# Performance work log

Measured on AMD Instinct MI355X. Metric: run time of the kernel, lower is better.

The kernel has to match this reference:

```python
import jax, jax.numpy as jnp
import numpy as np

N_HEADS = 16


def setup_inputs() -> dict:
    key = jax.random.key(0)
    k1, k2, k3, k4 = jax.random.split(key, 4)
    B, T, C = 2, 2048, 1024
    x = jax.random.normal(k1, (B, T, C), dtype=jnp.float32)
    scale = 1.0 / np.sqrt(C)
    Wq = jax.random.normal(k2, (C, C), dtype=jnp.float32) * scale
    Wk = jax.random.normal(k3, (C, C), dtype=jnp.float32) * scale
    Wv = jax.random.normal(k4, (C, C), dtype=jnp.float32) * scale
    return {"x": x, "Wq": Wq, "Wk": Wk, "Wv": Wv}


def reference(x, Wq, Wk, Wv):
    B, T, C = x.shape
    H = N_HEADS
    Dh = C // H
    # Faithful to original: direct view of (B,T,C) -> (B,H,T,Dh) (no transpose)
    q = (x @ Wq.T).reshape(B, H, T, Dh)
    k = (x @ Wk.T).reshape(B, H, T, Dh)
    v = (x @ Wv.T).reshape(B, H, T, Dh)
    scores = jnp.einsum('bhqd,bhkd->bhqk', q, k) * (1.0 / (Dh ** 0.5))
    mask = jnp.tril(jnp.ones((T, T), dtype=bool))  # causal mask
    scores = jnp.where(mask, scores, -jnp.inf)
    att = jax.nn.softmax(scores, axis=-1)
    out = jnp.einsum('bhqk,bhkd->bhqd', att, v)
    return out.reshape(B, T, C)
```

## Files before the change

### kernel.cpp

```cpp
#include <hip/hip_runtime.h>
#include <hip/hip_bf16.h>
#include <stdint.h>

#define AS1 __attribute__((address_space(1)))
#define AS3 __attribute__((address_space(3)))

typedef __bf16 bf16x8 __attribute__((ext_vector_type(8)));
typedef float  f32x4  __attribute__((ext_vector_type(4)));
typedef unsigned short ushort8v __attribute__((ext_vector_type(8)));
typedef unsigned short ushort4v __attribute__((ext_vector_type(4)));
typedef short short8v __attribute__((ext_vector_type(8)));
typedef short short4v __attribute__((ext_vector_type(4)));

__device__ __forceinline__ unsigned short f2bf(float f) {
    unsigned int u = __float_as_uint(f);
    u += 0x7fffu + ((u >> 16) & 1u);
    return (unsigned short)(u >> 16);
}
__device__ __forceinline__ unsigned int pk2bf(float a, float b) {
    __hip_bfloat162 h = __float22bfloat162_rn(make_float2(a, b));
    unsigned int u;
    __builtin_memcpy(&u, &h, 4);
    return u;
}
__device__ __forceinline__ void g2lds16(const void* gp, void* lp) {
    __builtin_amdgcn_global_load_lds((AS1 void*)gp, (AS3 void*)lp, 16, 0, 0);
}
#define E2(x) __builtin_amdgcn_exp2f(x)

__global__ __launch_bounds__(256) void cast_all(const float* __restrict__ x,
                                                const float* __restrict__ w0,
                                                const float* __restrict__ w1,
                                                const float* __restrict__ w2,
                                                unsigned short* __restrict__ xb,
                                                unsigned short* __restrict__ wc) {
    int id = blockIdx.x;
    const float* s;
    unsigned short* d;
    int base;
    if (id < 4096) { s = x; d = xb; base = id; }
    else {
        int z = (id - 4096) >> 10;
        s = (z == 0) ? w0 : (z == 1) ? w1 : w2;
        d = wc + (size_t)z * 1048576;
        base = (id - 4096) & 1023;
    }
    int i = (base * 256 + threadIdx.x) * 4;
    float4 v = *(const float4*)(s + i);
    ushort4v o = { f2bf(v.x), f2bf(v.y), f2bf(v.z), f2bf(v.w) };
    *(ushort4v*)(d + i) = o;
}

__global__ __launch_bounds__(256) void gemm_qkv(const unsigned short* __restrict__ X,
                                                const unsigned short* __restrict__ W,
                                                unsigned short* __restrict__ QKV) {
    const int K = 1024, N = 1024;
    const int z = blockIdx.z;
    const unsigned short* A = X;
    const unsigned short* B = W + (size_t)z * (1024 * 1024);
    unsigned short* C = QKV + (size_t)z * (4096 * 1024);
    const float qs = (z == 0) ? 0.18033688011112042f : 1.0f;

    const int m0 = blockIdx.y * 128;
    const int n0 = blockIdx.x * 128;

    __shared__ unsigned short As[128 * 32];
    __shared__ unsigned short Bs[128 * 32];

    const int t = threadIdx.x;
    const int w = t >> 6;
    const int l = t & 63;
    const int wm = (w >> 1) * 64;
    const int wn = (w & 1) * 64;
    const int cl = l & 15;
    const int quad = l >> 4;

    const int srow = w * 16 + (l >> 2);
    const int scol = (l & 3) * 8;

    f32x4 acc[4][4] = {};

    for (int k0 = 0; k0 < K; k0 += 32) {
        g2lds16(A + (size_t)(m0 + srow) * K + k0 + scol,      As + w * 512);
        g2lds16(A + (size_t)(m0 + 64 + srow) * K + k0 + scol, As + 2048 + w * 512);
        g2lds16(B + (size_t)(n0 + srow) * K + k0 + scol,      Bs + w * 512);
        g2lds16(B + (size_t)(n0 + 64 + srow) * K + k0 + scol, Bs + 2048 + w * 512);
        __syncthreads();

        bf16x8 af[4], bfr[4];
        #pragma unroll
        for (int i = 0; i < 4; ++i)
            af[i] = *(const bf16x8*)(As + (wm + i * 16 + cl) * 32 + quad * 8);
        #pragma unroll
        for (int j = 0; j < 4; ++j)
            bfr[j] = *(const bf16x8*)(Bs + (wn + j * 16 + cl) * 32 + quad * 8);
        #pragma unroll
        for (int i = 0; i < 4; ++i)
            #pragma unroll
            for (int j = 0; j < 4; ++j)
                acc[i][j] = __builtin_amdgcn_mfma_f32_16x16x32_bf16(af[i], bfr[j], acc[i][j], 0, 0, 0);
        __syncthreads();
    }

    #pragma unroll
    for (int i = 0; i < 4; ++i) {
        #pragma unroll
        for (int r = 0; r < 4; ++r) {
            size_t row = (size_t)(m0 + wm + i * 16 + quad * 4 + r);
            #pragma unroll
            for (int j = 0; j < 4; ++j)
                C[row * N + (n0 + wn + j * 16 + cl)] = f2bf(acc[i][j][r] * qs);
        }
    }
}

__global__ __launch_bounds__(256) void vtrans(const unsigned short* __restrict__ Vn,
                                              unsigned short* __restrict__ V3) {
    const int bh = blockIdx.y;
    const int T0 = blockIdx.x * 128;
    __shared__ unsigned short L[128 * 72];
    const int t = threadIdx.x;

    const unsigned short* src = Vn + (size_t)bh * 131072 + (size_t)T0 * 64;
    #pragma unroll
    for (int p = 0; p < 4; ++p) {
        int r = p * 32 + (t >> 3), c = (t & 7) * 8;
        *(ushort8v*)(L + r * 72 + c) = *(const ushort8v*)(src + (size_t)r * 64 + c);
    }
    __syncthreads();
    unsigned short* dst = V3 + (size_t)bh * 131072 + (size_t)(T0 >> 4) * 1024;
    #pragma unroll
    for (int p = 0; p < 2; ++p) {
        int item = p * 256 + t;
        int kb = item >> 6, cl = (item >> 2) & 15, qk = item & 3;
        ushort8v a, b;
        #pragma unroll
        for (int u = 0; u < 8; ++u) {
            int dt = u >> 2, j = u & 3;
            a[u] = L[(kb * 16 + qk * 4 + j) * 72 + dt * 16 + cl];
            b[u] = L[(kb * 16 + qk * 4 + j) * 72 + (dt + 2) * 16 + cl];
        }
        unsigned short* dp = dst + kb * 1024 + cl * 64 + qk * 16;
        *(ushort8v*)(dp) = a;
        *(ushort8v*)(dp + 8) = b;
    }
}

__global__ __launch_bounds__(256) void attn(const unsigned short* __restrict__ QK,
                                            const unsigned short* __restrict__ V3,
                                            float* __restrict__ Out) {
    const int id = blockIdx.x;
    const int bh = (id & 7) * 4 + ((id >> 3) & 3);
    const int pp = id >> 5;
    const int t = threadIdx.x;
    const int w = t >> 6;
    const int l = t & 63;
    const int cl = l & 15;
    const int quad = l >> 4;
    const int c7 = cl & 7;

    const size_t bhoff = (size_t)bh * 131072;
    const unsigned short* Qb = QK + bhoff;
    const unsigned short* Kb = QK + (size_t)4194304 + bhoff;
    const unsigned short* Vb = V3 + bhoff;
    float* Ob = Out + bhoff;

    __shared__ unsigned short KVs[2][8192];

    const int sg0 = t, sg1 = 256 + t;
    const int kO0 = (sg0 >> 3) * 64 + (((sg0 & 7) ^ ((sg0 >> 3) & 7)) * 8);
    const int kO1 = (sg1 >> 3) * 64 + (((sg1 & 7) ^ ((sg1 >> 3) & 7)) * 8);
    const int wg0 = sg0 & 63, wg1 = sg1 & 63;
    const int vO0 = (sg0 >> 6) * 512 + ((wg0 ^ ((wg0 >> 3) & 7)) * 8);
    const int vO1 = (sg1 >> 6) * 512 + ((wg1 ^ ((wg1 >> 3) & 7)) * 8);
    const int lB0 = w * 512;
    const int lB1 = 2048 + w * 512;

    const int oK0 = cl * 64 + (((quad)     ^ c7) * 8);
    const int oK1 = cl * 64 + (((quad + 4) ^ c7) * 8);
    const int oV0 = cl * 64 + (((quad * 2)     ^ c7) * 8);
    const int oV1 = cl * 64 + (((quad * 2 + 1) ^ c7) * 8);

    const int mrel = w * 16 + cl;

    #pragma unroll 1
    for (int hb = 0; hb < 2; ++hb) {
        const int bb = hb ? (31 - pp) : pp;
        const int m0 = bb * 64 + w * 16;
        const int nch = bb + 1;

        bf16x8 qf0, qf1;
        {
            const unsigned short* qa = Qb + (size_t)(m0 + cl) * 64 + quad * 8;
            qf0 = *(const bf16x8*)(qa);
            qf1 = *(const bf16x8*)(qa + 32);
        }

        f32x4 o[4] = {};
        float lps = 0.f;

        {
            unsigned short* s = &KVs[0][0];
            g2lds16(Kb + kO0, s + lB0);
            g2lds16(Kb + kO1, s + lB1);
            g2lds16(Vb + vO0, s + 4096 + lB0);
            g2lds16(Vb + vO1, s + 4096 + lB1);
        }

        for (int c = 0; c < nch; ++c) {
            __syncthreads();
            if (c + 1 < nch) {
                const unsigned short* kg = Kb + (size_t)(c + 1) * 4096;
                const unsigned short* vg = Vb + (size_t)(c + 1) * 4096;
                unsigned short* s = &KVs[(c + 1) & 1][0];
                g2lds16(kg + kO0, s + lB0);
                g2lds16(kg + kO1, s + lB1);
                g2lds16(vg + vO0, s + 4096 + lB0);
                g2lds16(vg + vO1, s + 4096 + lB1);
            }
            const unsigned short* Kl = &KVs[c & 1][0];
            const unsigned short* Vl = Kl + 4096;
            const bool masked = (c == nch - 1) && (hb == 0 ? true : true) && (c == bb);

            bf16x8 kf0[4], kf1[4];
            #pragma unroll
            for (int kt = 0; kt < 4; ++kt) {
                kf0[kt] = *(const bf16x8*)(Kl + kt * 1024 + oK0);
                kf1[kt] = *(const bf16x8*)(Kl + kt * 1024 + oK1);
            }
            f32x4 st[4] = {};
            #pragma unroll
            for (int kt = 0; kt < 4; ++kt) {
                st[kt] = __builtin_amdgcn_mfma_f32_16x16x32_bf16(kf0[kt], qf0, st[kt], 0, 0, 0);
                st[kt] = __builtin_amdgcn_mfma_f32_16x16x32_bf16(kf1[kt], qf1, st[kt], 0, 0, 0);
            }

            short4v pb[4];
            #pragma unroll
            for (int kt = 0; kt < 4; ++kt) {
                float p0, p1, p2, p3;
                if (masked) {
                    const int lk = kt * 16 + quad * 4;
                    p0 = (lk     <= mrel) ? E2(st[kt][0]) : 0.f;
                    p1 = (lk + 1 <= mrel) ? E2(st[kt][1]) : 0.f;
                    p2 = (lk + 2 <= mrel) ? E2(st[kt][2]) : 0.f;
                    p3 = (lk + 3 <= mrel) ? E2(st[kt][3]) : 0.f;
                } else {
                    p0 = E2(st[kt][0]);
                    p1 = E2(st[kt][1]);
                    p2 = E2(st[kt][2]);
                    p3 = E2(st[kt][3]);
                }
                lps += (p0 + p1) + (p2 + p3);
                uint2 u = { pk2bf(p0, p1), pk2bf(p2, p3) };
                short4v pv;
                __builtin_memcpy(&pv, &u, 8);
                pb[kt] = pv;
            }

            #pragma unroll
            for (int kt = 0; kt < 4; ++kt) {
                short8v v0 = *(const short8v*)(Vl + kt * 1024 + oV0);
                short8v v1 = *(const short8v*)(Vl + kt * 1024 + oV1);
                short4v a0 = __builtin_shufflevector(v0, v0, 0, 1, 2, 3);
                short4v a1 = __builtin_shufflevector(v0, v0, 4, 5, 6, 7);
                short4v a2 = __builtin_shufflevector(v1, v1, 0, 1, 2, 3);
                short4v a3 = __builtin_shufflevector(v1, v1, 4, 5, 6, 7);
                o[0] = __builtin_amdgcn_mfma_f32_16x16x16bf16_1k(a0, pb[kt], o[0], 0, 0, 0);
                o[1] = __builtin_amdgcn_mfma_f32_16x16x16bf16_1k(a1, pb[kt], o[1], 0, 0, 0);
                o[2] = __builtin_amdgcn_mfma_f32_16x16x16bf16_1k(a2, pb[kt], o[2], 0, 0, 0);
                o[3] = __builtin_amdgcn_mfma_f32_16x16x16bf16_1k(a3, pb[kt], o[3], 0, 0, 0);
            }
        }
        __syncthreads();

        lps += __shfl_xor(lps, 16);
        lps += __shfl_xor(lps, 32);
        const float inv = 1.0f / lps;
        #pragma unroll
        for (int dt = 0; dt < 4; ++dt) {
            f32x4 r = o[dt];
            r[0] *= inv; r[1] *= inv; r[2] *= inv; r[3] *= inv;
            *(f32x4*)(Ob + (size_t)(m0 + cl) * 64 + dt * 16 + quad * 4) = r;
        }
    }
}

extern "C" void kernel_launch(void* const* d_in, const int* in_sizes, int n_in,
                              void* d_out, int out_size, void* d_ws, size_t ws_size,
                              hipStream_t stream) {
    const float* x  = (const float*)d_in[0];
    const float* Wq = (const float*)d_in[1];
    const float* Wk = (const float*)d_in[2];
    const float* Wv = (const float*)d_in[3];
    float* out = (float*)d_out;

    unsigned short* xb  = (unsigned short*)d_ws;
    unsigned short* wc  = xb + (size_t)4096 * 1024;
    unsigned short* qkv = wc + (size_t)3 * 1024 * 1024;
    unsigned short* vt  = qkv + (size_t)3 * 4096 * 1024;

    hipLaunchKernelGGL(cast_all, dim3(7168), dim3(256), 0, stream, x, Wq, Wk, Wv, xb, wc);
    hipLaunchKernelGGL(gemm_qkv, dim3(8, 32, 3), dim3(256), 0, stream, xb, wc, qkv);
    hipLaunchKernelGGL(vtrans, dim3(16, 32), dim3(256), 0, stream, qkv + (size_t)2 * 4096 * 1024, vt);
    hipLaunchKernelGGL(attn, dim3(512), dim3(256), 0, stream, qkv, vt, out);
}
```

Measured before the change: 148.0 us.

## Double-buffer QKV GEMM with swizzled LDS and share K/V tiles across paired query blocks

The QKV GEMM now double-buffers its LDS tiles, prefetching the next K slice while computing the current one, and XOR-swizzles the LDS column layout to cut bank conflicts. This drops one barrier per iteration. The attention kernel no longer walks K/V twice for its two paired query blocks (short and long). It loads each K/V chunk once and computes both blocks against it, roughly halving K/V loads and barriers. The cost is more registers for two accumulator sets, which may lower occupancy.

```diff
diff --git a/kernel.cpp b/kernel.cpp
--- a/kernel.cpp
+++ b/kernel.cpp
@@ -64,8 +64,8 @@
     const int m0 = blockIdx.y * 128;
     const int n0 = blockIdx.x * 128;
 
-    __shared__ unsigned short As[128 * 32];
-    __shared__ unsigned short Bs[128 * 32];
+    __shared__ unsigned short As[2][128 * 32];
+    __shared__ unsigned short Bs[2][128 * 32];
 
     const int t = threadIdx.x;
     const int w = t >> 6;
@@ -76,30 +76,42 @@
     const int quad = l >> 4;
 
     const int srow = w * 16 + (l >> 2);
-    const int scol = (l & 3) * 8;
+    const int scol = ((l & 3) ^ ((l >> 2) & 3)) * 8;
+    const int rsw = (cl & 3);
 
     f32x4 acc[4][4] = {};
 
-    for (int k0 = 0; k0 < K; k0 += 32) {
-        g2lds16(A + (size_t)(m0 + srow) * K + k0 + scol,      As + w * 512);
-        g2lds16(A + (size_t)(m0 + 64 + srow) * K + k0 + scol, As + 2048 + w * 512);
-        g2lds16(B + (size_t)(n0 + srow) * K + k0 + scol,      Bs + w * 512);
-        g2lds16(B + (size_t)(n0 + 64 + srow) * K + k0 + scol, Bs + 2048 + w * 512);
+    g2lds16(A + (size_t)(m0 + srow) * K + scol,      &As[0][w * 512]);
+    g2lds16(A + (size_t)(m0 + 64 + srow) * K + scol, &As[0][2048 + w * 512]);
+    g2lds16(B + (size_t)(n0 + srow) * K + scol,      &Bs[0][w * 512]);
+    g2lds16(B + (size_t)(n0 + 64 + srow) * K + scol, &Bs[0][2048 + w * 512]);
+
+    for (int kc = 0; kc < 32; ++kc) {
         __syncthreads();
+        if (kc + 1 < 32) {
+            const int k0 = (kc + 1) * 32;
+            unsigned short* a = &As[(kc + 1) & 1][0];
+            unsigned short* b = &Bs[(kc + 1) & 1][0];
+            g2lds16(A + (size_t)(m0 + srow) * K + k0 + scol,      a + w * 512);
+            g2lds16(A + (size_t)(m0 + 64 + srow) * K + k0 + scol, a + 2048 + w * 512);
+            g2lds16(B + (size_t)(n0 + srow) * K + k0 + scol,      b + w * 512);
+            g2lds16(B + (size_t)(n0 + 64 + srow) * K + k0 + scol, b + 2048 + w * 512);
+        }
+        const unsigned short* Al = &As[kc & 1][0];
+        const unsigned short* Bl = &Bs[kc & 1][0];
 
         bf16x8 af[4], bfr[4];
         #pragma unroll
         for (int i = 0; i < 4; ++i)
-            af[i] = *(const bf16x8*)(As + (wm + i * 16 + cl) * 32 + quad * 8);
+            af[i] = *(const bf16x8*)(Al + (wm + i * 16 + cl) * 32 + ((quad ^ rsw) * 8));
         #pragma unroll
         for (int j = 0; j < 4; ++j)
-            bfr[j] = *(const bf16x8*)(Bs + (wn + j * 16 + cl) * 32 + quad * 8);
+            bfr[j] = *(const bf16x8*)(Bl + (wn + j * 16 + cl) * 32 + ((quad ^ rsw) * 8));
         #pragma unroll
         for (int i = 0; i < 4; ++i)
             #pragma unroll
             for (int j = 0; j < 4; ++j)
                 acc[i][j] = __builtin_amdgcn_mfma_f32_16x16x32_bf16(af[i], bfr[j], acc[i][j], 0, 0, 0);
-        __syncthreads();
     }
 
     #pragma unroll
@@ -183,106 +195,146 @@
 
     const int mrel = w * 16 + cl;
 
-    #pragma unroll 1
-    for (int hb = 0; hb < 2; ++hb) {
-        const int bb = hb ? (31 - pp) : pp;
-        const int m0 = bb * 64 + w * 16;
-        const int nch = bb + 1;
-
-        bf16x8 qf0, qf1;
+    const int bL = 31 - pp;
+    const int nchL = 32 - pp;
+    const int m0L = bL * 64 + w * 16;
+    const int m0S = pp * 64 + w * 16;
+
+    bf16x8 qfL0, qfL1, qfS0, qfS1;
+    {
+        const unsigned short* qa = Qb + (size_t)(m0L + cl) * 64 + quad * 8;
+        qfL0 = *(const bf16x8*)(qa);
+        qfL1 = *(const bf16x8*)(qa + 32);
+        const unsigned short* qs = Qb + (size_t)(m0S + cl) * 64 + quad * 8;
+        qfS0 = *(const bf16x8*)(qs);
+        qfS1 = *(const bf16x8*)(qs + 32);
+    }
+
+    f32x4 oL[4] = {}, oS[4] = {};
+    float lpL = 0.f, lpS = 0.f;
+
+    {
+        unsigned short* s = &KVs[0][0];
+        g2lds16(Kb + kO0, s + lB0);
+        g2lds16(Kb + kO1, s + lB1);
+        g2lds16(Vb + vO0, s + 4096 + lB0);
+        g2lds16(Vb + vO1, s + 4096 + lB1);
+    }
+
+    for (int c = 0; c < nchL; ++c) {
+        __syncthreads();
+        if (c + 1 < nchL) {
+            const unsigned short* kg = Kb + (size_t)(c + 1) * 4096;
+            const unsigned short* vg = Vb + (size_t)(c + 1) * 4096;
+            unsigned short* s = &KVs[(c + 1) & 1][0];
+            g2lds16(kg + kO0, s + lB0);
+            g2lds16(kg + kO1, s + lB1);
+            g2lds16(vg + vO0, s + 4096 + lB0);
+            g2lds16(vg + vO1, s + 4096 + lB1);
+        }
+        const unsigned short* Kl = &KVs[c & 1][0];
+        const unsigned short* Vl = Kl + 4096;
+        const bool doS = (c <= pp);
+
+        bf16x8 kf0[4], kf1[4];
+        #pragma unroll
+        for (int kt = 0; kt < 4; ++kt) {
+            kf0[kt] = *(const bf16x8*)(Kl + kt * 1024 + oK0);
+            kf1[kt] = *(const bf16x8*)(Kl + kt * 1024 + oK1);
+        }
+
+        f32x4 stL[4] = {};
+        #pragma unroll
+        for (int kt = 0; kt < 4; ++kt) {
+            stL[kt] = __builtin_amdgcn_mfma_f32_16x16x32_bf16(kf0[kt], qfL0, stL[kt], 0, 0, 0);
+            stL[kt] = __builtin_amdgcn_mfma_f32_16x16x32_bf16(kf1[kt], qfL1, stL[kt], 0, 0, 0);
+        }
+        f32x4 stS[4] = {};
+        if (doS) {
+            #pragma unroll
+            for (int kt = 0; kt < 4; ++kt) {
+                stS[kt] = __builtin_amdgcn_mfma_f32_16x16x32_bf16(kf0[kt], qfS0, stS[kt], 0, 0, 0);
+                stS[kt] = __builtin_amdgcn_mfma_f32_16x16x32_bf16(kf1[kt], qfS1, stS[kt], 0, 0, 0);
+            }
+        }
+
+        short4v pbL[4], pbS[4];
         {
-            const unsigned short* qa = Qb + (size_t)(m0 + cl) * 64 + quad * 8;
-            qf0 = *(const bf16x8*)(qa);
-            qf1 = *(const bf16x8*)(qa + 32);
-        }
-
-        f32x4 o[4] = {};
-        float lps = 0.f;
-
-        {
-            unsigned short* s = &KVs[0][0];
-            g2lds16(Kb + kO0, s + lB0);
-            g2lds16(Kb + kO1, s + lB1);
-            g2lds16(Vb + vO0, s + 4096 + lB0);
-            g2lds16(Vb + vO1, s + 4096 + lB1);
-        }
-
-        for (int c = 0; c < nch; ++c) {
-            __syncthreads();
-            if (c + 1 < nch) {
-                const unsigned short* kg = Kb + (size_t)(c + 1) * 4096;
-                const unsigned short* vg = Vb + (size_t)(c + 1) * 4096;
-                unsigned short* s = &KVs[(c + 1) & 1][0];
-                g2lds16(kg + kO0, s + lB0);
-                g2lds16(kg + kO1, s + lB1);
-                g2lds16(vg + vO0, s + 4096 + lB0);
-                g2lds16(vg + vO1, s + 4096 + lB1);
-            }
-            const unsigned short* Kl = &KVs[c & 1][0];
-            const unsigned short* Vl = Kl + 4096;
-            const bool masked = (c == nch - 1) && (hb == 0 ? true : true) && (c == bb);
-
-            bf16x8 kf0[4], kf1[4];
-            #pragma unroll
-            for (int kt = 0; kt < 4; ++kt) {
-                kf0[kt] = *(const bf16x8*)(Kl + kt * 1024 + oK0);
-                kf1[kt] = *(const bf16x8*)(Kl + kt * 1024 + oK1);
-            }
-            f32x4 st[4] = {};
-            #pragma unroll
-            for (int kt = 0; kt < 4; ++kt) {
-                st[kt] = __builtin_amdgcn_mfma_f32_16x16x32_bf16(kf0[kt], qf0, st[kt], 0, 0, 0);
-                st[kt] = __builtin_amdgcn_mfma_f32_16x16x32_bf16(kf1[kt], qf1, st[kt], 0, 0, 0);
-            }
-
-            short4v pb[4];
+            const bool mL = (c == nchL - 1);
             #pragma unroll
             for (int kt = 0; kt < 4; ++kt) {
                 float p0, p1, p2, p3;
-                if (masked) {
+                if (mL) {
                     const int lk = kt * 16 + quad * 4;
-                    p0 = (lk     <= mrel) ? E2(st[kt][0]) : 0.f;
-                    p1 = (lk + 1 <= mrel) ? E2(st[kt][1]) : 0.f;
-                    p2 = (lk + 2 <= mrel) ? E2(st[kt][2]) : 0.f;
-                    p3 = (lk + 3 <= mrel) ? E2(st[kt][3]) : 0.f;
+                    p0 = (lk     <= mrel) ? E2(stL[kt][0]) : 0.f;
+                    p1 = (lk + 1 <= mrel) ? E2(stL[kt][1]) : 0.f;
+                    p2 = (lk + 2 <= mrel) ? E2(stL[kt][2]) : 0.f;
+                    p3 = (lk + 3 <= mrel) ? E2(stL[kt][3]) : 0.f;
                 } else {
-                    p0 = E2(st[kt][0]);
-                    p1 = E2(st[kt][1]);
-                    p2 = E2(st[kt][2]);
-                    p3 = E2(st[kt][3]);
+                    p0 = E2(stL[kt][0]); p1 = E2(stL[kt][1]);
+                    p2 = E2(stL[kt][2]); p3 = E2(stL[kt][3]);
                 }
-                lps += (p0 + p1) + (p2 + p3);
+                lpL += (p0 + p1) + (p2 + p3);
                 uint2 u = { pk2bf(p0, p1), pk2bf(p2, p3) };
-                short4v pv;
-                __builtin_memcpy(&pv, &u, 8);
-                pb[kt] = pv;
+                __builtin_memcpy(&pbL[kt], &u, 8);
             }
-
+        }
+        if (doS) {
+            const bool mS = (c == pp);
             #pragma unroll
             for (int kt = 0; kt < 4; ++kt) {
-                short8v v0 = *(const short8v*)(Vl + kt * 1024 + oV0);
-                short8v v1 = *(const short8v*)(Vl + kt * 1024 + oV1);
-                short4v a0 = __builtin_shufflevector(v0, v0, 0, 1, 2, 3);
-                short4v a1 = __builtin_shufflevector(v0, v0, 4, 5, 6, 7);
-                short4v a2 = __builtin_shufflevector(v1, v1, 0, 1, 2, 3);
-                short4v a3 = __builtin_shufflevector(v1, v1, 4, 5, 6, 7);
-                o[0] = __builtin_amdgcn_mfma_f32_16x16x16bf16_1k(a0, pb[kt], o[0], 0, 0, 0);
-                o[1] = __builtin_amdgcn_mfma_f32_16x16x16bf16_1k(a1, pb[kt], o[1], 0, 0, 0);
-                o[2] = __builtin_amdgcn_mfma_f32_16x16x16bf16_1k(a2, pb[kt], o[2], 0, 0, 0);
-                o[3] = __builtin_amdgcn_mfma_f32_16x16x16bf16_1k(a3, pb[kt], o[3], 0, 0, 0);
+                float p0, p1, p2, p3;
+                if (mS) {
+                    const int lk = kt * 16 + quad * 4;
+                    p0 = (lk     <= mrel) ? E2(stS[kt][0]) : 0.f;
+                    p1 = (lk + 1 <= mrel) ? E2(stS[kt][1]) : 0.f;
+                    p2 = (lk + 2 <= mrel) ? E2(stS[kt][2]) : 0.f;
+                    p3 = (lk + 3 <= mrel) ? E2(stS[kt][3]) : 0.f;
+                } else {
+                    p0 = E2(stS[kt][0]); p1 = E2(stS[kt][1]);
+                    p2 = E2(stS[kt][2]); p3 = E2(stS[kt][3]);
+                }
+                lpS += (p0 + p1) + (p2 + p3);
+                uint2 u = { pk2bf(p0, p1), pk2bf(p2, p3) };
+                __builtin_memcpy(&pbS[kt], &u, 8);
             }
         }
-        __syncthreads();
-
-        lps += __shfl_xor(lps, 16);
-        lps += __shfl_xor(lps, 32);
-        const float inv = 1.0f / lps;
-        #pragma unroll
-        for (int dt = 0; dt < 4; ++dt) {
-            f32x4 r = o[dt];
-            r[0] *= inv; r[1] *= inv; r[2] *= inv; r[3] *= inv;
-            *(f32x4*)(Ob + (size_t)(m0 + cl) * 64 + dt * 16 + quad * 4) = r;
-        }
+
+        #pragma unroll
+        for (int kt = 0; kt < 4; ++kt) {
+            short8v v0 = *(const short8v*)(Vl + kt * 1024 + oV0);
+            short8v v1 = *(const short8v*)(Vl + kt * 1024 + oV1);
+            short4v a0 = __builtin_shufflevector(v0, v0, 0, 1, 2, 3);
+            short4v a1 = __builtin_shufflevector(v0, v0, 4, 5, 6, 7);
+            short4v a2 = __builtin_shufflevector(v1, v1, 0, 1, 2, 3);
+            short4v a3 = __builtin_shufflevector(v1, v1, 4, 5, 6, 7);
+            oL[0] = __builtin_amdgcn_mfma_f32_16x16x16bf16_1k(a0, pbL[kt], oL[0], 0, 0, 0);
+            oL[1] = __builtin_amdgcn_mfma_f32_16x16x16bf16_1k(a1, pbL[kt], oL[1], 0, 0, 0);
+            oL[2] = __builtin_amdgcn_mfma_f32_16x16x16bf16_1k(a2, pbL[kt], oL[2], 0, 0, 0);
+            oL[3] = __builtin_amdgcn_mfma_f32_16x16x16bf16_1k(a3, pbL[kt], oL[3], 0, 0, 0);
+            if (doS) {
+                oS[0] = __builtin_amdgcn_mfma_f32_16x16x16bf16_1k(a0, pbS[kt], oS[0], 0, 0, 0);
+                oS[1] = __builtin_amdgcn_mfma_f32_16x16x16bf16_1k(a1, pbS[kt], oS[1], 0, 0, 0);
+                oS[2] = __builtin_amdgcn_mfma_f32_16x16x16bf16_1k(a2, pbS[kt], oS[2], 0, 0, 0);
+                oS[3] = __builtin_amdgcn_mfma_f32_16x16x16bf16_1k(a3, pbS[kt], oS[3], 0, 0, 0);
+            }
+        }
+    }
+
+    lpL += __shfl_xor(lpL, 16);
+    lpL += __shfl_xor(lpL, 32);
+    lpS += __shfl_xor(lpS, 16);
+    lpS += __shfl_xor(lpS, 32);
+    const float invL = 1.0f / lpL;
+    const float invS = 1.0f / lpS;
+    #pragma unroll
+    for (int dt = 0; dt < 4; ++dt) {
+        f32x4 r = oL[dt];
+        r[0] *= invL; r[1] *= invL; r[2] *= invL; r[3] *= invL;
+        *(f32x4*)(Ob + (size_t)(m0L + cl) * 64 + dt * 16 + quad * 4) = r;
+        f32x4 q = oS[dt];
+        q[0] *= invS; q[1] *= invS; q[2] *= invS; q[3] *= invS;
+        *(f32x4*)(Ob + (size_t)(m0S + cl) * 64 + dt * 16 + quad * 4) = q;
     }
 }
 
```

Measured after the change: 159.6 us. +7.8%, slower.

## Enlarge attention query tile to 128 rows per block with two M-tiles per wave

Applied to the files above, without the earlier changes.

Each attention block now processes 128 query rows (each wave handles two 16-row tiles) instead of 64, so each K/V chunk loaded into LDS is reused across twice as many queries. The grid is halved to 256 blocks and waves whose rows end earlier skip the trailing causal chunk. This reduces K/V global-to-LDS traffic and barrier count per query. The costs are higher register pressure, fewer blocks for the CUs, and some waves idling on the last chunk.

```diff
diff --git a/kernel.cpp b/kernel.cpp
--- a/kernel.cpp
+++ b/kernel.cpp
@@ -181,23 +181,25 @@
     const int oV0 = cl * 64 + (((quad * 2)     ^ c7) * 8);
     const int oV1 = cl * 64 + (((quad * 2 + 1) ^ c7) * 8);
 
-    const int mrel = w * 16 + cl;
+    const int mloc = 32 * (w & 1);
 
     #pragma unroll 1
     for (int hb = 0; hb < 2; ++hb) {
-        const int bb = hb ? (31 - pp) : pp;
-        const int m0 = bb * 64 + w * 16;
-        const int nch = bb + 1;
-
-        bf16x8 qf0, qf1;
-        {
-            const unsigned short* qa = Qb + (size_t)(m0 + cl) * 64 + quad * 8;
-            qf0 = *(const bf16x8*)(qa);
-            qf1 = *(const bf16x8*)(qa + 32);
-        }
-
-        f32x4 o[4] = {};
-        float lps = 0.f;
+        const int bb = hb ? (15 - pp) : pp;
+        const int nchB = 2 * bb + 2;
+        const int myLast = 2 * bb + (w >> 1);
+        const int m0w = bb * 128 + w * 32;
+
+        bf16x8 qf[2][2];
+        #pragma unroll
+        for (int mt = 0; mt < 2; ++mt) {
+            const unsigned short* qa = Qb + (size_t)(m0w + mt * 16 + cl) * 64 + quad * 8;
+            qf[mt][0] = *(const bf16x8*)(qa);
+            qf[mt][1] = *(const bf16x8*)(qa + 32);
+        }
+
+        f32x4 o[2][4] = {};
+        float lp[2] = {0.f, 0.f};
 
         {
             unsigned short* s = &KVs[0][0];
@@ -207,9 +209,9 @@
             g2lds16(Vb + vO1, s + 4096 + lB1);
         }
 
-        for (int c = 0; c < nch; ++c) {
+        for (int c = 0; c < nchB; ++c) {
             __syncthreads();
-            if (c + 1 < nch) {
+            if (c + 1 < nchB) {
                 const unsigned short* kg = Kb + (size_t)(c + 1) * 4096;
                 const unsigned short* vg = Vb + (size_t)(c + 1) * 4096;
                 unsigned short* s = &KVs[(c + 1) & 1][0];
@@ -218,9 +220,10 @@
                 g2lds16(vg + vO0, s + 4096 + lB0);
                 g2lds16(vg + vO1, s + 4096 + lB1);
             }
+            if (c > myLast) continue;
             const unsigned short* Kl = &KVs[c & 1][0];
             const unsigned short* Vl = Kl + 4096;
-            const bool masked = (c == nch - 1) && (hb == 0 ? true : true) && (c == bb);
+            const bool masked = (c == myLast);
 
             bf16x8 kf0[4], kf1[4];
             #pragma unroll
@@ -228,34 +231,39 @@
                 kf0[kt] = *(const bf16x8*)(Kl + kt * 1024 + oK0);
                 kf1[kt] = *(const bf16x8*)(Kl + kt * 1024 + oK1);
             }
-            f32x4 st[4] = {};
-            #pragma unroll
-            for (int kt = 0; kt < 4; ++kt) {
-                st[kt] = __builtin_amdgcn_mfma_f32_16x16x32_bf16(kf0[kt], qf0, st[kt], 0, 0, 0);
-                st[kt] = __builtin_amdgcn_mfma_f32_16x16x32_bf16(kf1[kt], qf1, st[kt], 0, 0, 0);
-            }
-
-            short4v pb[4];
-            #pragma unroll
-            for (int kt = 0; kt < 4; ++kt) {
-                float p0, p1, p2, p3;
-                if (masked) {
-                    const int lk = kt * 16 + quad * 4;
-                    p0 = (lk     <= mrel) ? E2(st[kt][0]) : 0.f;
-                    p1 = (lk + 1 <= mrel) ? E2(st[kt][1]) : 0.f;
-                    p2 = (lk + 2 <= mrel) ? E2(st[kt][2]) : 0.f;
-                    p3 = (lk + 3 <= mrel) ? E2(st[kt][3]) : 0.f;
-                } else {
-                    p0 = E2(st[kt][0]);
-                    p1 = E2(st[kt][1]);
-                    p2 = E2(st[kt][2]);
-                    p3 = E2(st[kt][3]);
+
+            f32x4 st[2][4] = {};
+            #pragma unroll
+            for (int mt = 0; mt < 2; ++mt)
+                #pragma unroll
+                for (int kt = 0; kt < 4; ++kt) {
+                    st[mt][kt] = __builtin_amdgcn_mfma_f32_16x16x32_bf16(kf0[kt], qf[mt][0], st[mt][kt], 0, 0, 0);
+                    st[mt][kt] = __builtin_amdgcn_mfma_f32_16x16x32_bf16(kf1[kt], qf[mt][1], st[mt][kt], 0, 0, 0);
                 }
-                lps += (p0 + p1) + (p2 + p3);
-                uint2 u = { pk2bf(p0, p1), pk2bf(p2, p3) };
-                short4v pv;
-                __builtin_memcpy(&pv, &u, 8);
-                pb[kt] = pv;
+
+            short4v pb[2][4];
+            #pragma unroll
+            for (int mt = 0; mt < 2; ++mt) {
+                const int mrel = mloc + mt * 16 + cl;
+                #pragma unroll
+                for (int kt = 0; kt < 4; ++kt) {
+                    float p0, p1, p2, p3;
+                    if (masked) {
+                        const int lk = kt * 16 + quad * 4;
+                        p0 = (lk     <= mrel) ? E2(st[mt][kt][0]) : 0.f;
+                        p1 = (lk + 1 <= mrel) ? E2(st[mt][kt][1]) : 0.f;
+                        p2 = (lk + 2 <= mrel) ? E2(st[mt][kt][2]) : 0.f;
+                        p3 = (lk + 3 <= mrel) ? E2(st[mt][kt][3]) : 0.f;
+                    } else {
+                        p0 = E2(st[mt][kt][0]);
+                        p1 = E2(st[mt][kt][1]);
+                        p2 = E2(st[mt][kt][2]);
+                        p3 = E2(st[mt][kt][3]);
+                    }
+                    lp[mt] += (p0 + p1) + (p2 + p3);
+                    uint2 u = { pk2bf(p0, p1), pk2bf(p2, p3) };
+                    __builtin_memcpy(&pb[mt][kt], &u, 8);
+                }
             }
 
             #pragma unroll
@@ -266,22 +274,29 @@
                 short4v a1 = __builtin_shufflevector(v0, v0, 4, 5, 6, 7);
                 short4v a2 = __builtin_shufflevector(v1, v1, 0, 1, 2, 3);
                 short4v a3 = __builtin_shufflevector(v1, v1, 4, 5, 6, 7);
-                o[0] = __builtin_amdgcn_mfma_f32_16x16x16bf16_1k(a0, pb[kt], o[0], 0, 0, 0);
-                o[1] = __builtin_amdgcn_mfma_f32_16x16x16bf16_1k(a1, pb[kt], o[1], 0, 0, 0);
-                o[2] = __builtin_amdgcn_mfma_f32_16x16x16bf16_1k(a2, pb[kt], o[2], 0, 0, 0);
-                o[3] = __builtin_amdgcn_mfma_f32_16x16x16bf16_1k(a3, pb[kt], o[3], 0, 0, 0);
+                #pragma unroll
+                for (int mt = 0; mt < 2; ++mt) {
+                    o[mt][0] = __builtin_amdgcn_mfma_f32_16x16x16bf16_1k(a0, pb[mt][kt], o[mt][0], 0, 0, 0);
+                    o[mt][1] = __builtin_amdgcn_mfma_f32_16x16x16bf16_1k(a1, pb[mt][kt], o[mt][1], 0, 0, 0);
+                    o[mt][2] = __builtin_amdgcn_mfma_f32_16x16x16bf16_1k(a2, pb[mt][kt], o[mt][2], 0, 0, 0);
+                    o[mt][3] = __builtin_amdgcn_mfma_f32_16x16x16bf16_1k(a3, pb[mt][kt], o[mt][3], 0, 0, 0);
+                }
             }
         }
         __syncthreads();
 
-        lps += __shfl_xor(lps, 16);
-        lps += __shfl_xor(lps, 32);
-        const float inv = 1.0f / lps;
-        #pragma unroll
-        for (int dt = 0; dt < 4; ++dt) {
-            f32x4 r = o[dt];
-            r[0] *= inv; r[1] *= inv; r[2] *= inv; r[3] *= inv;
-            *(f32x4*)(Ob + (size_t)(m0 + cl) * 64 + dt * 16 + quad * 4) = r;
+        #pragma unroll
+        for (int mt = 0; mt < 2; ++mt) {
+            float s = lp[mt];
+            s += __shfl_xor(s, 16);
+            s += __shfl_xor(s, 32);
+            const float inv = 1.0f / s;
+            #pragma unroll
+            for (int dt = 0; dt < 4; ++dt) {
+                f32x4 r = o[mt][dt];
+                r[0] *= inv; r[1] *= inv; r[2] *= inv; r[3] *= inv;
+                *(f32x4*)(Ob + (size_t)(m0w + mt * 16 + cl) * 64 + dt * 16 + quad * 4) = r;
+            }
         }
     }
 }
@@ -303,5 +318,5 @@
     hipLaunchKernelGGL(cast_all, dim3(7168), dim3(256), 0, stream, x, Wq, Wk, Wv, xb, wc);
     hipLaunchKernelGGL(gemm_qkv, dim3(8, 32, 3), dim3(256), 0, stream, xb, wc, qkv);
     hipLaunchKernelGGL(vtrans, dim3(16, 32), dim3(256), 0, stream, qkv + (size_t)2 * 4096 * 1024, vt);
-    hipLaunchKernelGGL(attn, dim3(512), dim3(256), 0, stream, qkv, vt, out);
-}
+    hipLaunchKernelGGL(attn, dim3(256), dim3(256), 0, stream, qkv, vt, out);
+}
```

Result: slower. 156.2 us (+5.5%).

## Double attention query tile to 128 rows with 512-thread blocks sharing K/V loads

Applied to the files above, without the earlier changes.

The attention kernel now runs 512 threads (8 waves) per block and covers 128 query rows instead of 64. Each K/V chunk in LDS therefore serves twice as many waves, and the grid shrinks from 512 to 256 blocks. Waves owning the lower 64 rows skip the final chunk past their causal limit. The aim is to halve K/V global traffic per query row, at the cost of fewer blocks, coarser causal load balancing and idle waves on the last chunk.

```diff
diff --git a/kernel.cpp b/kernel.cpp
--- a/kernel.cpp
+++ b/kernel.cpp
@@ -146,7 +146,7 @@
     }
 }
 
-__global__ __launch_bounds__(256) void attn(const unsigned short* __restrict__ QK,
+__global__ __launch_bounds__(512) void attn(const unsigned short* __restrict__ QK,
                                             const unsigned short* __restrict__ V3,
                                             float* __restrict__ Out) {
     const int id = blockIdx.x;
@@ -167,31 +167,29 @@
 
     __shared__ unsigned short KVs[2][8192];
 
-    const int sg0 = t, sg1 = 256 + t;
-    const int kO0 = (sg0 >> 3) * 64 + (((sg0 & 7) ^ ((sg0 >> 3) & 7)) * 8);
-    const int kO1 = (sg1 >> 3) * 64 + (((sg1 & 7) ^ ((sg1 >> 3) & 7)) * 8);
-    const int wg0 = sg0 & 63, wg1 = sg1 & 63;
-    const int vO0 = (sg0 >> 6) * 512 + ((wg0 ^ ((wg0 >> 3) & 7)) * 8);
-    const int vO1 = (sg1 >> 6) * 512 + ((wg1 ^ ((wg1 >> 3) & 7)) * 8);
-    const int lB0 = w * 512;
-    const int lB1 = 2048 + w * 512;
+    const int sg = t;
+    const int kO = (sg >> 3) * 64 + (((sg & 7) ^ ((sg >> 3) & 7)) * 8);
+    const int wg = sg & 63;
+    const int vO = (sg >> 6) * 512 + ((wg ^ ((wg >> 3) & 7)) * 8);
+    const int lB = w * 512;
 
     const int oK0 = cl * 64 + (((quad)     ^ c7) * 8);
     const int oK1 = cl * 64 + (((quad + 4) ^ c7) * 8);
     const int oV0 = cl * 64 + (((quad * 2)     ^ c7) * 8);
     const int oV1 = cl * 64 + (((quad * 2 + 1) ^ c7) * 8);
 
-    const int mrel = w * 16 + cl;
+    const int mrel = (w & 3) * 16 + cl;
 
     #pragma unroll 1
     for (int hb = 0; hb < 2; ++hb) {
-        const int bb = hb ? (31 - pp) : pp;
-        const int m0 = bb * 64 + w * 16;
-        const int nch = bb + 1;
+        const int bb = hb ? (15 - pp) : pp;
+        const int nchB = 2 * bb + 2;
+        const int myLast = 2 * bb + (w >> 2);
+        const int m0w = bb * 128 + w * 16;
 
         bf16x8 qf0, qf1;
         {
-            const unsigned short* qa = Qb + (size_t)(m0 + cl) * 64 + quad * 8;
+            const unsigned short* qa = Qb + (size_t)(m0w + cl) * 64 + quad * 8;
             qf0 = *(const bf16x8*)(qa);
             qf1 = *(const bf16x8*)(qa + 32);
         }
@@ -201,26 +199,21 @@
 
         {
             unsigned short* s = &KVs[0][0];
-            g2lds16(Kb + kO0, s + lB0);
-            g2lds16(Kb + kO1, s + lB1);
-            g2lds16(Vb + vO0, s + 4096 + lB0);
-            g2lds16(Vb + vO1, s + 4096 + lB1);
-        }
-
-        for (int c = 0; c < nch; ++c) {
+            g2lds16(Kb + kO, s + lB);
+            g2lds16(Vb + vO, s + 4096 + lB);
+        }
+
+        for (int c = 0; c < nchB; ++c) {
             __syncthreads();
-            if (c + 1 < nch) {
-                const unsigned short* kg = Kb + (size_t)(c + 1) * 4096;
-                const unsigned short* vg = Vb + (size_t)(c + 1) * 4096;
+            if (c + 1 < nchB) {
                 unsigned short* s = &KVs[(c + 1) & 1][0];
-                g2lds16(kg + kO0, s + lB0);
-                g2lds16(kg + kO1, s + lB1);
-                g2lds16(vg + vO0, s + 4096 + lB0);
-                g2lds16(vg + vO1, s + 4096 + lB1);
-            }
+                g2lds16(Kb + (size_t)(c + 1) * 4096 + kO, s + lB);
+                g2lds16(Vb + (size_t)(c + 1) * 4096 + vO, s + 4096 + lB);
+            }
+            if (c > myLast) continue;
             const unsigned short* Kl = &KVs[c & 1][0];
             const unsigned short* Vl = Kl + 4096;
-            const bool masked = (c == nch - 1) && (hb == 0 ? true : true) && (c == bb);
+            const bool masked = (c == myLast);
 
             bf16x8 kf0[4], kf1[4];
             #pragma unroll
@@ -281,7 +274,7 @@
         for (int dt = 0; dt < 4; ++dt) {
             f32x4 r = o[dt];
             r[0] *= inv; r[1] *= inv; r[2] *= inv; r[3] *= inv;
-            *(f32x4*)(Ob + (size_t)(m0 + cl) * 64 + dt * 16 + quad * 4) = r;
+            *(f32x4*)(Ob + (size_t)(m0w + cl) * 64 + dt * 16 + quad * 4) = r;
         }
     }
 }
@@ -303,5 +296,5 @@
     hipLaunchKernelGGL(cast_all, dim3(7168), dim3(256), 0, stream, x, Wq, Wk, Wv, xb, wc);
     hipLaunchKernelGGL(gemm_qkv, dim3(8, 32, 3), dim3(256), 0, stream, xb, wc, qkv);
     hipLaunchKernelGGL(vtrans, dim3(16, 32), dim3(256), 0, stream, qkv + (size_t)2 * 4096 * 1024, vt);
-    hipLaunchKernelGGL(attn, dim3(512), dim3(256), 0, stream, qkv, vt, out);
-}
+    hipLaunchKernelGGL(attn, dim3(256), dim3(512), 0, stream, qkv, vt, out);
+}
```

After: 148.2 us, median of 2. No clear change (+0.2%).
